# Kernel optimization log

Measured on AMD Instinct MI355X. Metric: run time of the kernel, lower is better.

## Reference

```python
import jax, jax.numpy as jnp
import numpy as np
from jax import lax

# 8-neighbor zero-pad offsets as (left, right, top, bottom), matching nn.ZeroPad2d args
PADS = [(0, 2, 0, 2), (1, 1, 0, 2), (2, 0, 0, 2), (0, 2, 1, 1),
        (2, 0, 1, 1), (0, 2, 2, 0), (1, 1, 2, 0), (2, 0, 2, 0)]
BN_EPS = 1e-5


def conv2d(x, w, pad):
    return lax.conv_general_dilated(x, w, (1, 1), [(pad, pad), (pad, pad)],
                                    dimension_numbers=('NCHW', 'OIHW', 'NCHW'))


def batchnorm(x, gamma, beta, mean, var):
    inv = gamma * lax.rsqrt(var + BN_EPS)
    return x * inv[None, :, None, None] + (beta - mean * inv)[None, :, None, None]


def resize_bilinear(x, oh, ow):
    # F.interpolate(mode='bilinear', align_corners=False)
    n, c, h, w = x.shape
    ys = jnp.clip((jnp.arange(oh, dtype=x.dtype) + 0.5) * (h / oh) - 0.5, 0.0, None)
    xs = jnp.clip((jnp.arange(ow, dtype=x.dtype) + 0.5) * (w / ow) - 0.5, 0.0, None)
    y0 = jnp.floor(ys); x0 = jnp.floor(xs)
    wy = (ys - y0)[:, None]; wx = (xs - x0)[None, :]
    y0i = jnp.clip(y0.astype(jnp.int32), 0, h - 1)
    y1i = jnp.clip(y0i + 1, 0, h - 1)
    x0i = jnp.clip(x0.astype(jnp.int32), 0, w - 1)
    x1i = jnp.clip(x0i + 1, 0, w - 1)
    r0 = x[:, :, y0i, :]; r1 = x[:, :, y1i, :]
    top = r0[:, :, :, x0i] * (1 - wx) + r0[:, :, :, x1i] * wx
    bot = r1[:, :, :, x0i] * (1 - wx) + r1[:, :, :, x1i] * wx
    return top * (1 - wy) + bot * wy


def lrwarp_error(left, disp, right):
    # Warp right image toward left using horizontal disparity (bilinear,
    # zero padding outside), then per-channel absolute photometric error.
    n, c, h, w = right.shape
    xs = jnp.arange(w, dtype=disp.dtype)[None, None, None, :] - disp  # [n,1,h,w]
    x0 = jnp.floor(xs)
    frac = xs - x0
    x0i = x0.astype(jnp.int32)
    x1i = x0i + 1
    v0 = ((x0i >= 0) & (x0i < w)).astype(right.dtype)
    v1 = ((x1i >= 0) & (x1i < w)).astype(right.dtype)
    x0c = jnp.broadcast_to(jnp.clip(x0i, 0, w - 1), (n, c, h, w))
    x1c = jnp.broadcast_to(jnp.clip(x1i, 0, w - 1), (n, c, h, w))
    g0 = jnp.take_along_axis(right, x0c, axis=3) * v0
    g1 = jnp.take_along_axis(right, x1c, axis=3) * v1
    warped = g0 * (1 - frac) + g1 * frac
    return jnp.abs(left - warped)


def setup_inputs() -> dict:
    key = jax.random.key(0)
    ks = jax.random.split(key, 16)
    N, H, W = 8, 256, 256
    inp = {
        'normal_estimation': jax.random.normal(ks[0], (N, 3, H, W), jnp.float32),
        'left_image': jax.random.uniform(ks[1], (N, 3, 512, 512), jnp.float32),
        'right_image': jax.random.uniform(ks[2], (N, 3, 512, 512), jnp.float32),
        'coarse_disparity': jax.random.uniform(ks[3], (N, 1, H, W), jnp.float32),
        'w1': jax.random.normal(ks[4], (32, 12, 3, 3), jnp.float32) * 0.1,
        'g1': jnp.ones((32,), jnp.float32), 'b1': jnp.zeros((32,), jnp.float32),
        'm1': jax.random.normal(ks[5], (32,), jnp.float32) * 0.01,
        'v1': jax.random.uniform(ks[6], (32,), jnp.float32, 0.5, 1.5),
        'w2': jax.random.normal(ks[7], (64, 32, 3, 3), jnp.float32) * 0.1,
        'g2': jnp.ones((64,), jnp.float32), 'b2': jnp.zeros((64,), jnp.float32),
        'm2': jax.random.normal(ks[8], (64,), jnp.float32) * 0.01,
        'v2': jax.random.uniform(ks[9], (64,), jnp.float32, 0.5, 1.5),
        'w3': jax.random.normal(ks[10], (8, 64, 1, 1), jnp.float32) * 0.1,
    }
    return inp


def _forward(normal_estimation, left_image, right_image, coarse_disparity,
             w1, g1, b1, m1, v1, w2, g2, b2, m2, v2, w3):
    H, W = coarse_disparity.shape[-2], coarse_disparity.shape[-1]
    cur_l = resize_bilinear(left_image, H, W)
    cur_r = resize_bilinear(right_image, H, W)
    disp_err = lrwarp_error(cur_l, coarse_disparity, cur_r)
    feats = jnp.concatenate([normal_estimation, cur_l, cur_r, disp_err], axis=1)
    x = jax.nn.relu(batchnorm(conv2d(feats, w1, 1), g1, b1, m1, v1))
    x = jax.nn.relu(batchnorm(conv2d(x, w2, 1), g2, b2, m2, v2))
    aff = jax.nn.relu(conv2d(x, w3, 0))  # [N,8,H,W]
    gate_p = jnp.stack([jnp.pad(aff[:, k], ((0, 0), (t, b), (l, r)))
                        for k, (l, r, t, b) in enumerate(PADS)], axis=1)
    d = coarse_disparity[:, 0]
    disp_p = jnp.stack([jnp.pad(d, ((0, 0), (t, b), (l, r)))
                        for (l, r, t, b) in PADS], axis=1)
    gate = jax.nn.softmax(gate_p, axis=1)
    prop = jnp.sum(gate * disp_p, axis=1, keepdims=True)[:, :, 1:-1, 1:-1]
    return prop * 0.3 + coarse_disparity * 0.7


def reference(normal_estimation, left_image, right_image, coarse_disparity,
              w1, g1, b1, m1, v1, w2, g2, b2, m2, v2, w3):
    return _forward(normal_estimation, left_image, right_image, coarse_disparity,
                    w1, g1, b1, m1, v1, w2, g2, b2, m2, v2, w3)
```

## Files before the change

kernel.cpp:

```cpp
#include <hip/hip_runtime.h>
#include <math.h>

#define NB 8
#define HH 256
#define WW 256
#define HW (HH*WW)

#define OFF_AFFB  0UL
#define OFF_W1FB  8388608UL
#define OFF_B1FB  8400896UL
#define OFF_W2FB  8401024UL
#define OFF_B2FB  8437888UL
#define OFF_W3FB  8438144UL

typedef short  short8 __attribute__((ext_vector_type(8)));
typedef ushort u16x8  __attribute__((ext_vector_type(8)));
typedef ushort u16x4  __attribute__((ext_vector_type(4)));
typedef float  f32x4  __attribute__((ext_vector_type(4)));

__device__ __forceinline__ ushort f2bf(float x) {
  uint u = __float_as_uint(x);
  return (ushort)((u + 0x7FFFu + ((u >> 16) & 1u)) >> 16);
}
__device__ __forceinline__ float bf2f(ushort h) {
  uint u = ((uint)h) << 16;
  return __uint_as_float(u);
}

__global__ __launch_bounds__(256) void prep_weights(
    const float* __restrict__ w1, const float* __restrict__ g1,
    const float* __restrict__ b1, const float* __restrict__ m1,
    const float* __restrict__ v1,
    const float* __restrict__ w2, const float* __restrict__ g2,
    const float* __restrict__ b2, const float* __restrict__ m2,
    const float* __restrict__ v2, const float* __restrict__ w3,
    char* __restrict__ wsb) {
  int idx = blockIdx.x * 256 + threadIdx.x;
  ushort* w1f = (ushort*)(wsb + OFF_W1FB);
  float* b1f  = (float*)(wsb + OFF_B1FB);
  ushort* w2f = (ushort*)(wsb + OFF_W2FB);
  float* b2f  = (float*)(wsb + OFF_B2FB);
  ushort* w3f = (ushort*)(wsb + OFF_W3FB);
  if (idx < 6144) {
    int jj = idx & 7;
    int lane = (idx >> 3) & 63;
    int nt = (idx >> 9) & 1;
    int s = idx >> 10;
    int ky = s >> 1, t = s & 1;
    int q = lane >> 4, lx = lane & 15;
    int k = q * 8 + jj;
    int dcol = k >> 4, ch = k & 15;
    int kx = t * 2 + dcol;
    int out = nt * 16 + lx;
    float inv = g1[out] / sqrtf(v1[out] + 1e-5f);
    float val = (ch < 12 && kx < 3) ? w1[((out * 12 + ch) * 3 + ky) * 3 + kx] * inv : 0.f;
    w1f[idx] = f2bf(val);
  }
  int j = idx - 6144;
  if (j >= 0 && j < 18432) {
    int kk   = j >> 11;
    int nt   = (j >> 9) & 3;
    int lane = (j >> 3) & 63;
    int jj   = j & 7;
    int q  = lane >> 4, lx = lane & 15;
    int cin = q * 8 + jj;
    int out = nt * 16 + lx;
    float inv = g2[out] / sqrtf(v2[out] + 1e-5f);
    w2f[j] = f2bf(w2[(out * 32 + cin) * 9 + kk] * inv);
    if (kk == 0 && q == 0 && jj == 0) b2f[out] = b2[out] - m2[out] * inv;
  }
  int k2 = idx - 24576;
  if (k2 >= 0 && k2 < 32) {
    float inv = g1[k2] / sqrtf(v1[k2] + 1e-5f);
    b1f[k2] = b1[k2] - m1[k2] * inv;
  }
  int k3 = idx - 24608;
  if (k3 >= 0 && k3 < 1024) {
    int jj = k3 & 7;
    int lane = (k3 >> 3) & 63;
    int slice = k3 >> 9;
    int q = lane >> 4, lx = lane & 15;
    int ch = slice * 32 + q * 8 + jj;
    w3f[k3] = (lx < 8) ? f2bf(w3[lx * 64 + ch]) : (ushort)0;
  }
}

__global__ __launch_bounds__(256) void trunk_kernel(
    const float* __restrict__ normal, const float* __restrict__ left,
    const float* __restrict__ right, const float* __restrict__ disp,
    char* __restrict__ wsb) {
  __shared__ ushort buf[18304];
  ushort* x1t = buf + 6464;
  const short8* __restrict__ w1fv = (const short8*)(wsb + OFF_W1FB);
  const float* __restrict__ b1f = (const float*)(wsb + OFF_B1FB);
  const short8* __restrict__ w2fv = (const short8*)(wsb + OFF_W2FB);
  const float* __restrict__ b2f = (const float*)(wsb + OFF_B2FB);
  const short8* __restrict__ w3fv = (const short8*)(wsb + OFF_W3FB);
  ushort* aff = (ushort*)(wsb + OFF_AFFB);

  int blk = blockIdx.x;
  int n = blk >> 8;
  int t = blk & 255;
  int ty0 = (t >> 4) << 4;
  int tx0 = (t & 15) << 4;
  int tid = threadIdx.x;
  int lane = tid & 63;
  int wid = tid >> 6;
  int q = lane >> 4;
  int lx = lane & 15;

  if (tid < 8) *(u16x8*)&buf[(800 + tid) * 8] = (u16x8)0;
  for (int e = tid; e < 400; e += 256) {
    int row = e / 20, col = e - row * 20;
    int gy = ty0 + row - 2, gx = tx0 + col - 2;
    ushort tmp[16];
#pragma unroll
    for (int c = 12; c < 16; ++c) tmp[c] = 0;
    if (gy >= 0 && gy < HH && gx >= 0 && gx < WW) {
#pragma unroll
      for (int c = 0; c < 3; ++c)
        tmp[c] = f2bf(normal[(size_t)(n * 3 + c) * HW + gy * WW + gx]);
      int i2 = gy << 1, j2 = gx << 1;
      float cl[3];
#pragma unroll
      for (int c = 0; c < 3; ++c) {
        const float* Lp = left + ((size_t)(n * 3 + c) * 512 + i2) * 512 + j2;
        float2 a0 = *(const float2*)Lp;
        float2 a1 = *(const float2*)(Lp + 512);
        cl[c] = 0.25f * (a0.x + a0.y + a1.x + a1.y);
        tmp[3 + c] = f2bf(cl[c]);
        const float* Rp = right + ((size_t)(n * 3 + c) * 512 + i2) * 512 + j2;
        float2 b0 = *(const float2*)Rp;
        float2 b1v = *(const float2*)(Rp + 512);
        tmp[6 + c] = f2bf(0.25f * (b0.x + b0.y + b1v.x + b1v.y));
      }
      float d = disp[(size_t)n * HW + gy * WW + gx];
      float xs = (float)gx - d;
      float x0f = floorf(xs);
      float fr = xs - x0f;
      int ix0 = (int)x0f;
      int ix1 = ix0 + 1;
      float vm0 = (ix0 >= 0 && ix0 < WW) ? 1.f : 0.f;
      float vm1 = (ix1 >= 0 && ix1 < WW) ? 1.f : 0.f;
      int x0c = min(max(ix0, 0), WW - 1);
      int x1c = min(max(ix1, 0), WW - 1);
      bool adj = (x1c == x0c + 1);
      int xs2 = min(x0c + 1, WW - 1);
#pragma unroll
      for (int c = 0; c < 3; ++c) {
        const float* Rb = right + ((size_t)(n * 3 + c) * 512 + i2) * 512;
        float2 f0 = *(const float2*)(Rb + (x0c << 1));
        float2 f1 = *(const float2*)(Rb + (x0c << 1) + 512);
        float2 f2v = *(const float2*)(Rb + (xs2 << 1));
        float2 f3 = *(const float2*)(Rb + (xs2 << 1) + 512);
        float avg0 = 0.25f * (f0.x + f0.y + f1.x + f1.y);
        float avg1 = 0.25f * (f2v.x + f2v.y + f3.x + f3.y);
        float gg0 = avg0 * vm0;
        float gg1 = (adj ? avg1 : avg0) * vm1;
        float warped = gg0 * (1.f - fr) + gg1 * fr;
        tmp[9 + c] = f2bf(fabsf(cl[c] - warped));
      }
    } else {
#pragma unroll
      for (int c = 0; c < 12; ++c) tmp[c] = 0;
    }
    int G0 = e * 2, G1 = G0 + 1;
    int s0 = G0 ^ ((G0 >> 3) & 7);
    int s1 = G1 ^ ((G1 >> 3) & 7);
    *(u16x8*)&buf[s0 * 8] = *(u16x8*)&tmp[0];
    *(u16x8*)&buf[s1 * 8] = *(u16x8*)&tmp[8];
  }
  __syncthreads();

  {
    short8 bw1[6][2];
#pragma unroll
    for (int s = 0; s < 6; ++s)
#pragma unroll
      for (int nt = 0; nt < 2; ++nt) bw1[s][nt] = w1fv[(s * 2 + nt) * 64 + lane];
    float bias1[2] = {b1f[lx], b1f[16 + lx]};
    for (int m = wid; m < 21; m += 4) {
      int pidx = min(m * 16 + lx, 323);
      int oyr = pidx / 18, oxr = pidx - oyr * 18;
      f32x4 a1[2];
      a1[0] = (f32x4)0.f; a1[1] = (f32x4)0.f;
#pragma unroll
      for (int s = 0; s < 6; ++s) {
        int ky = s >> 1, tt = s & 1;
        int G = ((oyr + ky) * 20 + oxr + tt * 2 + (q >> 1)) * 2 + (q & 1);
        int slot = G ^ ((G >> 3) & 7);
        short8 a = *(const short8*)&buf[slot * 8];
        a1[0] = __builtin_amdgcn_mfma_f32_16x16x32_bf16(a, bw1[s][0], a1[0], 0, 0, 0);
        a1[1] = __builtin_amdgcn_mfma_f32_16x16x32_bf16(a, bw1[s][1], a1[1], 0, 0, 0);
      }
#pragma unroll
      for (int r = 0; r < 4; ++r) {
        int p2 = m * 16 + q * 4 + r;
        if (p2 < 324) {
          int ry = p2 / 18, rx = p2 - ry * 18;
          int gy = ty0 + ry - 1, gx = tx0 + rx - 1;
          bool okp = (gy >= 0 && gy < HH && gx >= 0 && gx < WW);
#pragma unroll
          for (int nt = 0; nt < 2; ++nt) {
            float v = okp ? fmaxf(a1[nt][r] + bias1[nt], 0.f) : 0.f;
            x1t[(ry * 18 + rx) * 36 + nt * 16 + lx] = f2bf(v);
          }
        }
      }
    }
  }
  __syncthreads();

  f32x4 acc[4][4];
#pragma unroll
  for (int mt = 0; mt < 4; ++mt)
#pragma unroll
    for (int nt = 0; nt < 4; ++nt) acc[mt][nt] = (f32x4)0.f;
#pragma unroll
  for (int kk = 0; kk < 9; ++kk) {
    int ky = kk / 3, kx = kk - ky * 3;
    short8 a[4], b[4];
#pragma unroll
    for (int mt = 0; mt < 4; ++mt) {
      int row = wid * 4 + mt;
      a[mt] = *(const short8*)&x1t[((row + ky) * 18 + lx + kx) * 36 + q * 8];
    }
#pragma unroll
    for (int nt = 0; nt < 4; ++nt) b[nt] = w2fv[(kk * 4 + nt) * 64 + lane];
#pragma unroll
    for (int mt = 0; mt < 4; ++mt)
#pragma unroll
      for (int nt = 0; nt < 4; ++nt)
        acc[mt][nt] = __builtin_amdgcn_mfma_f32_16x16x32_bf16(a[mt], b[nt], acc[mt][nt], 0, 0, 0);
  }
  __syncthreads();

#pragma unroll
  for (int nt = 0; nt < 4; ++nt) {
    float bias = b2f[nt * 16 + lx];
#pragma unroll
    for (int mt = 0; mt < 4; ++mt) {
      int row = wid * 4 + mt;
#pragma unroll
      for (int r = 0; r < 4; ++r) {
        int p = row * 16 + q * 4 + r;
        float v = fmaxf(acc[mt][nt][r] + bias, 0.f);
        buf[p * 68 + nt * 16 + lx] = f2bf(v);
      }
    }
  }
  __syncthreads();

  short8 bw3[2];
  bw3[0] = w3fv[lane];
  bw3[1] = w3fv[64 + lane];
  f32x4 acc3[4];
#pragma unroll
  for (int mt = 0; mt < 4; ++mt) acc3[mt] = (f32x4)0.f;
#pragma unroll
  for (int mt = 0; mt < 4; ++mt) {
    int p = wid * 64 + mt * 16 + lx;
#pragma unroll
    for (int s = 0; s < 2; ++s) {
      short8 a3 = *(const short8*)&buf[p * 68 + s * 32 + q * 8];
      acc3[mt] = __builtin_amdgcn_mfma_f32_16x16x32_bf16(a3, bw3[s], acc3[mt], 0, 0, 0);
    }
  }
  if (lx < 8) {
#pragma unroll
    for (int mt = 0; mt < 4; ++mt) {
      int py = ty0 + wid * 4 + mt;
      int px = tx0 + q * 4;
      u16x4 pk;
#pragma unroll
      for (int r = 0; r < 4; ++r) pk[r] = f2bf(fmaxf(acc3[mt][r], 0.f));
      *(u16x4*)&aff[((size_t)(n * 8 + lx)) * HW + (size_t)py * WW + px] = pk;
    }
  }
}

__global__ __launch_bounds__(256) void final_kernel(const float* __restrict__ disp,
                                                    const char* __restrict__ wsb,
                                                    float* __restrict__ out) {
  int gid = blockIdx.x * 256 + threadIdx.x;
  int n = gid >> 14;
  int r = gid & 16383;
  int i = r >> 6;
  int j0 = (r & 63) << 2;
  const ushort* aff = (const ushort*)(wsb + OFF_AFFB);
  float d6[3][6];
#pragma unroll
  for (int rr = 0; rr < 3; ++rr) {
    int y = min(max(i + rr - 1, 0), HH - 1);
    const float* dp = disp + (size_t)n * HW + y * WW;
    float4 c4 = *(const float4*)(dp + j0);
    d6[rr][1] = c4.x; d6[rr][2] = c4.y; d6[rr][3] = c4.z; d6[rr][4] = c4.w;
    d6[rr][0] = dp[max(j0 - 1, 0)];
    d6[rr][5] = dp[min(j0 + 4, WW - 1)];
  }
  const int dy[8] = {1, 1, 1, 0, 0, -1, -1, -1};
  const int dx[8] = {1, 0, -1, 1, -1, 1, 0, -1};
  float g[8][4], dvv[8][4];
#pragma unroll
  for (int k = 0; k < 8; ++k) {
    int y = i + dy[k];
    bool vy = (y >= 0 && y < HH);
    int yc = min(max(y, 0), HH - 1);
    const ushort* ap = aff + ((size_t)(n * 8 + k)) * HW + (size_t)yc * WW;
    float w6[6];
    u16x4 c4 = *(const u16x4*)(ap + j0);
    w6[1] = bf2f(c4[0]); w6[2] = bf2f(c4[1]); w6[3] = bf2f(c4[2]); w6[4] = bf2f(c4[3]);
    w6[0] = bf2f(ap[max(j0 - 1, 0)]);
    w6[5] = bf2f(ap[min(j0 + 4, WW - 1)]);
    int rr = dy[k] + 1;
#pragma unroll
    for (int p = 0; p < 4; ++p) {
      int xp = j0 + p + dx[k];
      bool ok = vy && (xp >= 0) && (xp < WW);
      g[k][p] = ok ? w6[p + 1 + dx[k]] : 0.f;
      dvv[k][p] = ok ? d6[rr][p + 1 + dx[k]] : 0.f;
    }
  }
  float4 res;
#pragma unroll
  for (int p = 0; p < 4; ++p) {
    float m = g[0][p];
#pragma unroll
    for (int k = 1; k < 8; ++k) m = fmaxf(m, g[k][p]);
    float se = 0.f, sed = 0.f;
#pragma unroll
    for (int k = 0; k < 8; ++k) {
      float e = __expf(g[k][p] - m);
      se += e;
      sed += e * dvv[k][p];
    }
    float dc = d6[1][p + 1];
    (&res.x)[p] = 0.3f * (sed / se) + 0.7f * dc;
  }
  *(float4*)(out + (size_t)n * HW + i * WW + j0) = res;
}

extern "C" void kernel_launch(void* const* d_in, const int* in_sizes, int n_in,
                              void* d_out, int out_size, void* d_ws, size_t ws_size,
                              hipStream_t stream) {
  const float* normal = (const float*)d_in[0];
  const float* left   = (const float*)d_in[1];
  const float* right  = (const float*)d_in[2];
  const float* disp   = (const float*)d_in[3];
  const float* w1 = (const float*)d_in[4];
  const float* g1 = (const float*)d_in[5];
  const float* b1 = (const float*)d_in[6];
  const float* m1 = (const float*)d_in[7];
  const float* v1 = (const float*)d_in[8];
  const float* w2 = (const float*)d_in[9];
  const float* g2 = (const float*)d_in[10];
  const float* b2 = (const float*)d_in[11];
  const float* m2 = (const float*)d_in[12];
  const float* v2 = (const float*)d_in[13];
  const float* w3 = (const float*)d_in[14];
  char* wsb  = (char*)d_ws;
  float* out = (float*)d_out;

  hipLaunchKernelGGL(prep_weights, dim3(101), dim3(256), 0, stream,
                     w1, g1, b1, m1, v1, w2, g2, b2, m2, v2, w3, wsb);
  hipLaunchKernelGGL(trunk_kernel, dim3(2048), dim3(256), 0, stream,
                     normal, left, right, disp, wsb);
  hipLaunchKernelGGL(final_kernel, dim3(512), dim3(256), 0, stream, disp, wsb, out);
}
```

Before: 169.0 us.

## Precompute downsampled images into packed pixel-major buffer before trunk kernel

A new pass merged into the weight-prep kernel computes the 2x2-averaged left/right images and packs them with normals and disparity into a 12-float-per-pixel interleaved workspace buffer. The trunk kernel then reads three float4 per pixel instead of re-averaging the full-resolution images, including for each halo pixel and each warp gather. The goal is to cut redundant full-resolution reads and strided per-channel gathers. In exchange it adds a full write and read of an intermediate buffer of about 25 MB.

```diff
diff --git a/kernel.cpp b/kernel.cpp
--- a/kernel.cpp
+++ b/kernel.cpp
@@ -12,6 +12,7 @@
 #define OFF_W2FB  8401024UL
 #define OFF_B2FB  8437888UL
 #define OFF_W3FB  8438144UL
+#define OFF_PACK  8440192UL
 
 typedef short  short8 __attribute__((ext_vector_type(8)));
 typedef ushort u16x8  __attribute__((ext_vector_type(8)));
@@ -27,7 +28,9 @@
   return __uint_as_float(u);
 }
 
-__global__ __launch_bounds__(256) void prep_weights(
+__global__ __launch_bounds__(256) void resize_pack(
+    const float* __restrict__ normal, const float* __restrict__ left,
+    const float* __restrict__ right, const float* __restrict__ disp,
     const float* __restrict__ w1, const float* __restrict__ g1,
     const float* __restrict__ b1, const float* __restrict__ m1,
     const float* __restrict__ v1,
@@ -35,60 +38,93 @@
     const float* __restrict__ b2, const float* __restrict__ m2,
     const float* __restrict__ v2, const float* __restrict__ w3,
     char* __restrict__ wsb) {
-  int idx = blockIdx.x * 256 + threadIdx.x;
-  ushort* w1f = (ushort*)(wsb + OFF_W1FB);
-  float* b1f  = (float*)(wsb + OFF_B1FB);
-  ushort* w2f = (ushort*)(wsb + OFF_W2FB);
-  float* b2f  = (float*)(wsb + OFF_B2FB);
-  ushort* w3f = (ushort*)(wsb + OFF_W3FB);
-  if (idx < 6144) {
-    int jj = idx & 7;
-    int lane = (idx >> 3) & 63;
-    int nt = (idx >> 9) & 1;
-    int s = idx >> 10;
-    int ky = s >> 1, t = s & 1;
-    int q = lane >> 4, lx = lane & 15;
-    int k = q * 8 + jj;
-    int dcol = k >> 4, ch = k & 15;
-    int kx = t * 2 + dcol;
-    int out = nt * 16 + lx;
-    float inv = g1[out] / sqrtf(v1[out] + 1e-5f);
-    float val = (ch < 12 && kx < 3) ? w1[((out * 12 + ch) * 3 + ky) * 3 + kx] * inv : 0.f;
-    w1f[idx] = f2bf(val);
-  }
-  int j = idx - 6144;
-  if (j >= 0 && j < 18432) {
-    int kk   = j >> 11;
-    int nt   = (j >> 9) & 3;
-    int lane = (j >> 3) & 63;
-    int jj   = j & 7;
-    int q  = lane >> 4, lx = lane & 15;
-    int cin = q * 8 + jj;
-    int out = nt * 16 + lx;
-    float inv = g2[out] / sqrtf(v2[out] + 1e-5f);
-    w2f[j] = f2bf(w2[(out * 32 + cin) * 9 + kk] * inv);
-    if (kk == 0 && q == 0 && jj == 0) b2f[out] = b2[out] - m2[out] * inv;
-  }
-  int k2 = idx - 24576;
-  if (k2 >= 0 && k2 < 32) {
-    float inv = g1[k2] / sqrtf(v1[k2] + 1e-5f);
-    b1f[k2] = b1[k2] - m1[k2] * inv;
-  }
-  int k3 = idx - 24608;
-  if (k3 >= 0 && k3 < 1024) {
-    int jj = k3 & 7;
-    int lane = (k3 >> 3) & 63;
-    int slice = k3 >> 9;
-    int q = lane >> 4, lx = lane & 15;
-    int ch = slice * 32 + q * 8 + jj;
-    w3f[k3] = (lx < 8) ? f2bf(w3[lx * 64 + ch]) : (ushort)0;
-  }
-}
-
-__global__ __launch_bounds__(256) void trunk_kernel(
-    const float* __restrict__ normal, const float* __restrict__ left,
-    const float* __restrict__ right, const float* __restrict__ disp,
-    char* __restrict__ wsb) {
+  if (blockIdx.x >= 1024) {
+    int idx = (blockIdx.x - 1024) * 256 + threadIdx.x;
+    ushort* w1f = (ushort*)(wsb + OFF_W1FB);
+    float* b1f  = (float*)(wsb + OFF_B1FB);
+    ushort* w2f = (ushort*)(wsb + OFF_W2FB);
+    float* b2f  = (float*)(wsb + OFF_B2FB);
+    ushort* w3f = (ushort*)(wsb + OFF_W3FB);
+    if (idx < 6144) {
+      int jj = idx & 7;
+      int lane = (idx >> 3) & 63;
+      int nt = (idx >> 9) & 1;
+      int s = idx >> 10;
+      int ky = s >> 1, t = s & 1;
+      int q = lane >> 4, lx = lane & 15;
+      int k = q * 8 + jj;
+      int dcol = k >> 4, ch = k & 15;
+      int kx = t * 2 + dcol;
+      int out = nt * 16 + lx;
+      float inv = g1[out] / sqrtf(v1[out] + 1e-5f);
+      float val = (ch < 12 && kx < 3) ? w1[((out * 12 + ch) * 3 + ky) * 3 + kx] * inv : 0.f;
+      w1f[idx] = f2bf(val);
+    }
+    int j = idx - 6144;
+    if (j >= 0 && j < 18432) {
+      int kk   = j >> 11;
+      int nt   = (j >> 9) & 3;
+      int lane = (j >> 3) & 63;
+      int jj   = j & 7;
+      int q  = lane >> 4, lx = lane & 15;
+      int cin = q * 8 + jj;
+      int out = nt * 16 + lx;
+      float inv = g2[out] / sqrtf(v2[out] + 1e-5f);
+      w2f[j] = f2bf(w2[(out * 32 + cin) * 9 + kk] * inv);
+      if (kk == 0 && q == 0 && jj == 0) b2f[out] = b2[out] - m2[out] * inv;
+    }
+    int k2 = idx - 24576;
+    if (k2 >= 0 && k2 < 32) {
+      float inv = g1[k2] / sqrtf(v1[k2] + 1e-5f);
+      b1f[k2] = b1[k2] - m1[k2] * inv;
+    }
+    int k3 = idx - 24608;
+    if (k3 >= 0 && k3 < 1024) {
+      int jj = k3 & 7;
+      int lane = (k3 >> 3) & 63;
+      int slice = k3 >> 9;
+      int q = lane >> 4, lx = lane & 15;
+      int ch = slice * 32 + q * 8 + jj;
+      w3f[k3] = (lx < 8) ? f2bf(w3[lx * 64 + ch]) : (ushort)0;
+    }
+    return;
+  }
+  int gid = blockIdx.x * 256 + threadIdx.x;
+  int n = gid >> 15;
+  int r = gid & 32767;
+  int i = r >> 7;
+  int j0 = (r & 127) << 1;
+  int i2 = i << 1;
+  float* pack = (float*)(wsb + OFF_PACK);
+  float rec[2][12];
+#pragma unroll
+  for (int c = 0; c < 3; ++c) {
+    const float* Lp = left + ((size_t)(n * 3 + c) * 512 + i2) * 512 + (j0 << 1);
+    float4 a0 = *(const float4*)Lp;
+    float4 a1 = *(const float4*)(Lp + 512);
+    rec[0][c] = 0.25f * (a0.x + a0.y + a1.x + a1.y);
+    rec[1][c] = 0.25f * (a0.z + a0.w + a1.z + a1.w);
+    const float* Rp = right + ((size_t)(n * 3 + c) * 512 + i2) * 512 + (j0 << 1);
+    float4 b0 = *(const float4*)Rp;
+    float4 b1v = *(const float4*)(Rp + 512);
+    rec[0][3 + c] = 0.25f * (b0.x + b0.y + b1v.x + b1v.y);
+    rec[1][3 + c] = 0.25f * (b0.z + b0.w + b1v.z + b1v.w);
+    float2 nm = *(const float2*)(normal + (size_t)(n * 3 + c) * HW + i * 256 + j0);
+    rec[0][6 + c] = nm.x;
+    rec[1][6 + c] = nm.y;
+  }
+  float2 dp2 = *(const float2*)(disp + (size_t)n * HW + i * 256 + j0);
+  rec[0][9] = dp2.x; rec[1][9] = dp2.y;
+  rec[0][10] = 0.f; rec[0][11] = 0.f; rec[1][10] = 0.f; rec[1][11] = 0.f;
+  float* ob = pack + ((size_t)(n * HW + i * 256 + j0)) * 12;
+#pragma unroll
+  for (int p = 0; p < 2; ++p)
+#pragma unroll
+    for (int vv = 0; vv < 3; ++vv)
+      *(float4*)(ob + p * 12 + vv * 4) = *(float4*)&rec[p][vv * 4];
+}
+
+__global__ __launch_bounds__(256) void trunk_kernel(char* __restrict__ wsb) {
   __shared__ ushort buf[18304];
   ushort* x1t = buf + 6464;
   const short8* __restrict__ w1fv = (const short8*)(wsb + OFF_W1FB);
@@ -96,6 +132,7 @@
   const short8* __restrict__ w2fv = (const short8*)(wsb + OFF_W2FB);
   const float* __restrict__ b2f = (const float*)(wsb + OFF_B2FB);
   const short8* __restrict__ w3fv = (const short8*)(wsb + OFF_W3FB);
+  const float* __restrict__ pack = (const float*)(wsb + OFF_PACK);
   ushort* aff = (ushort*)(wsb + OFF_AFFB);
 
   int blk = blockIdx.x;
@@ -117,24 +154,16 @@
 #pragma unroll
     for (int c = 12; c < 16; ++c) tmp[c] = 0;
     if (gy >= 0 && gy < HH && gx >= 0 && gx < WW) {
-#pragma unroll
-      for (int c = 0; c < 3; ++c)
-        tmp[c] = f2bf(normal[(size_t)(n * 3 + c) * HW + gy * WW + gx]);
-      int i2 = gy << 1, j2 = gx << 1;
-      float cl[3];
-#pragma unroll
-      for (int c = 0; c < 3; ++c) {
-        const float* Lp = left + ((size_t)(n * 3 + c) * 512 + i2) * 512 + j2;
-        float2 a0 = *(const float2*)Lp;
-        float2 a1 = *(const float2*)(Lp + 512);
-        cl[c] = 0.25f * (a0.x + a0.y + a1.x + a1.y);
-        tmp[3 + c] = f2bf(cl[c]);
-        const float* Rp = right + ((size_t)(n * 3 + c) * 512 + i2) * 512 + j2;
-        float2 b0 = *(const float2*)Rp;
-        float2 b1v = *(const float2*)(Rp + 512);
-        tmp[6 + c] = f2bf(0.25f * (b0.x + b0.y + b1v.x + b1v.y));
-      }
-      float d = disp[(size_t)n * HW + gy * WW + gx];
+      const float* P = pack + ((size_t)((n << 16) + gy * 256 + gx)) * 12;
+      float4 r0 = *(const float4*)P;
+      float4 r1 = *(const float4*)(P + 4);
+      float4 r2 = *(const float4*)(P + 8);
+      float cl[3] = {r0.x, r0.y, r0.z};
+      float cr[3] = {r0.w, r1.x, r1.y};
+      tmp[0] = f2bf(r1.z); tmp[1] = f2bf(r1.w); tmp[2] = f2bf(r2.x);
+      tmp[3] = f2bf(cl[0]); tmp[4] = f2bf(cl[1]); tmp[5] = f2bf(cl[2]);
+      tmp[6] = f2bf(cr[0]); tmp[7] = f2bf(cr[1]); tmp[8] = f2bf(cr[2]);
+      float d = r2.y;
       float xs = (float)gx - d;
       float x0f = floorf(xs);
       float fr = xs - x0f;
@@ -144,20 +173,11 @@
       float vm1 = (ix1 >= 0 && ix1 < WW) ? 1.f : 0.f;
       int x0c = min(max(ix0, 0), WW - 1);
       int x1c = min(max(ix1, 0), WW - 1);
-      bool adj = (x1c == x0c + 1);
-      int xs2 = min(x0c + 1, WW - 1);
+      const float* R0 = pack + ((size_t)((n << 16) + gy * 256 + x0c)) * 12 + 3;
+      const float* R1 = pack + ((size_t)((n << 16) + gy * 256 + x1c)) * 12 + 3;
 #pragma unroll
       for (int c = 0; c < 3; ++c) {
-        const float* Rb = right + ((size_t)(n * 3 + c) * 512 + i2) * 512;
-        float2 f0 = *(const float2*)(Rb + (x0c << 1));
-        float2 f1 = *(const float2*)(Rb + (x0c << 1) + 512);
-        float2 f2v = *(const float2*)(Rb + (xs2 << 1));
-        float2 f3 = *(const float2*)(Rb + (xs2 << 1) + 512);
-        float avg0 = 0.25f * (f0.x + f0.y + f1.x + f1.y);
-        float avg1 = 0.25f * (f2v.x + f2v.y + f3.x + f3.y);
-        float gg0 = avg0 * vm0;
-        float gg1 = (adj ? avg1 : avg0) * vm1;
-        float warped = gg0 * (1.f - fr) + gg1 * fr;
+        float warped = R0[c] * vm0 * (1.f - fr) + R1[c] * vm1 * fr;
         tmp[9 + c] = f2bf(fabsf(cl[c] - warped));
       }
     } else {
@@ -361,9 +381,9 @@
   char* wsb  = (char*)d_ws;
   float* out = (float*)d_out;
 
-  hipLaunchKernelGGL(prep_weights, dim3(101), dim3(256), 0, stream,
+  hipLaunchKernelGGL(resize_pack, dim3(1125), dim3(256), 0, stream,
+                     normal, left, right, disp,
                      w1, g1, b1, m1, v1, w2, g2, b2, m2, v2, w3, wsb);
-  hipLaunchKernelGGL(trunk_kernel, dim3(2048), dim3(256), 0, stream,
-                     normal, left, right, disp, wsb);
+  hipLaunchKernelGGL(trunk_kernel, dim3(2048), dim3(256), 0, stream, wsb);
   hipLaunchKernelGGL(final_kernel, dim3(512), dim3(256), 0, stream, disp, wsb, out);
 }
```

Measured after the change: 168.4 us. About the same (-0.4%).

## Precompute bf16 feature tensor in a row kernel fused with weight prep

Applied to the files above, without the earlier changes.

Adds a per-row kernel that computes the 12-channel input features (normal, downsampled left and right images, warp error) once per pixel and stores them as bf16 in workspace. Inside that kernel the warp gathers from a shared-memory row of the downsampled right image. The weight-prep blocks are appended to the same launch. The trunk kernel now loads its halo tile straight from this feature buffer instead of recomputing features with duplicated global gathers for every halo pixel. The cost is an extra write and read of the feature tensor plus a kernel boundary in place of the fused in-tile computation.

```diff
diff --git a/kernel.cpp b/kernel.cpp
--- a/kernel.cpp
+++ b/kernel.cpp
@@ -12,6 +12,7 @@
 #define OFF_W2FB  8401024UL
 #define OFF_B2FB  8437888UL
 #define OFF_W3FB  8438144UL
+#define OFF_FEATS 8440192UL
 
 typedef short  short8 __attribute__((ext_vector_type(8)));
 typedef ushort u16x8  __attribute__((ext_vector_type(8)));
@@ -27,7 +28,9 @@
   return __uint_as_float(u);
 }
 
-__global__ __launch_bounds__(256) void prep_weights(
+__global__ __launch_bounds__(256) void feats_row(
+    const float* __restrict__ normal, const float* __restrict__ left,
+    const float* __restrict__ right, const float* __restrict__ disp,
     const float* __restrict__ w1, const float* __restrict__ g1,
     const float* __restrict__ b1, const float* __restrict__ m1,
     const float* __restrict__ v1,
@@ -35,60 +38,109 @@
     const float* __restrict__ b2, const float* __restrict__ m2,
     const float* __restrict__ v2, const float* __restrict__ w3,
     char* __restrict__ wsb) {
-  int idx = blockIdx.x * 256 + threadIdx.x;
-  ushort* w1f = (ushort*)(wsb + OFF_W1FB);
-  float* b1f  = (float*)(wsb + OFF_B1FB);
-  ushort* w2f = (ushort*)(wsb + OFF_W2FB);
-  float* b2f  = (float*)(wsb + OFF_B2FB);
-  ushort* w3f = (ushort*)(wsb + OFF_W3FB);
-  if (idx < 6144) {
-    int jj = idx & 7;
-    int lane = (idx >> 3) & 63;
-    int nt = (idx >> 9) & 1;
-    int s = idx >> 10;
-    int ky = s >> 1, t = s & 1;
-    int q = lane >> 4, lx = lane & 15;
-    int k = q * 8 + jj;
-    int dcol = k >> 4, ch = k & 15;
-    int kx = t * 2 + dcol;
-    int out = nt * 16 + lx;
-    float inv = g1[out] / sqrtf(v1[out] + 1e-5f);
-    float val = (ch < 12 && kx < 3) ? w1[((out * 12 + ch) * 3 + ky) * 3 + kx] * inv : 0.f;
-    w1f[idx] = f2bf(val);
-  }
-  int j = idx - 6144;
-  if (j >= 0 && j < 18432) {
-    int kk   = j >> 11;
-    int nt   = (j >> 9) & 3;
-    int lane = (j >> 3) & 63;
-    int jj   = j & 7;
-    int q  = lane >> 4, lx = lane & 15;
-    int cin = q * 8 + jj;
-    int out = nt * 16 + lx;
-    float inv = g2[out] / sqrtf(v2[out] + 1e-5f);
-    w2f[j] = f2bf(w2[(out * 32 + cin) * 9 + kk] * inv);
-    if (kk == 0 && q == 0 && jj == 0) b2f[out] = b2[out] - m2[out] * inv;
-  }
-  int k2 = idx - 24576;
-  if (k2 >= 0 && k2 < 32) {
-    float inv = g1[k2] / sqrtf(v1[k2] + 1e-5f);
-    b1f[k2] = b1[k2] - m1[k2] * inv;
-  }
-  int k3 = idx - 24608;
-  if (k3 >= 0 && k3 < 1024) {
-    int jj = k3 & 7;
-    int lane = (k3 >> 3) & 63;
-    int slice = k3 >> 9;
-    int q = lane >> 4, lx = lane & 15;
-    int ch = slice * 32 + q * 8 + jj;
-    w3f[k3] = (lx < 8) ? f2bf(w3[lx * 64 + ch]) : (ushort)0;
-  }
-}
-
-__global__ __launch_bounds__(256) void trunk_kernel(
-    const float* __restrict__ normal, const float* __restrict__ left,
-    const float* __restrict__ right, const float* __restrict__ disp,
-    char* __restrict__ wsb) {
+  if (blockIdx.x >= 2048) {
+    int idx = (blockIdx.x - 2048) * 256 + threadIdx.x;
+    ushort* w1f = (ushort*)(wsb + OFF_W1FB);
+    float* b1f  = (float*)(wsb + OFF_B1FB);
+    ushort* w2f = (ushort*)(wsb + OFF_W2FB);
+    float* b2f  = (float*)(wsb + OFF_B2FB);
+    ushort* w3f = (ushort*)(wsb + OFF_W3FB);
+    if (idx < 6144) {
+      int jj = idx & 7;
+      int lane = (idx >> 3) & 63;
+      int nt = (idx >> 9) & 1;
+      int s = idx >> 10;
+      int ky = s >> 1, t = s & 1;
+      int q = lane >> 4, lx = lane & 15;
+      int k = q * 8 + jj;
+      int dcol = k >> 4, ch = k & 15;
+      int kx = t * 2 + dcol;
+      int out = nt * 16 + lx;
+      float inv = g1[out] / sqrtf(v1[out] + 1e-5f);
+      float val = (ch < 12 && kx < 3) ? w1[((out * 12 + ch) * 3 + ky) * 3 + kx] * inv : 0.f;
+      w1f[idx] = f2bf(val);
+    }
+    int j = idx - 6144;
+    if (j >= 0 && j < 18432) {
+      int kk   = j >> 11;
+      int nt   = (j >> 9) & 3;
+      int lane = (j >> 3) & 63;
+      int jj   = j & 7;
+      int q  = lane >> 4, lx = lane & 15;
+      int cin = q * 8 + jj;
+      int out = nt * 16 + lx;
+      float inv = g2[out] / sqrtf(v2[out] + 1e-5f);
+      w2f[j] = f2bf(w2[(out * 32 + cin) * 9 + kk] * inv);
+      if (kk == 0 && q == 0 && jj == 0) b2f[out] = b2[out] - m2[out] * inv;
+    }
+    int k2 = idx - 24576;
+    if (k2 >= 0 && k2 < 32) {
+      float inv = g1[k2] / sqrtf(v1[k2] + 1e-5f);
+      b1f[k2] = b1[k2] - m1[k2] * inv;
+    }
+    int k3 = idx - 24608;
+    if (k3 >= 0 && k3 < 1024) {
+      int jj = k3 & 7;
+      int lane = (k3 >> 3) & 63;
+      int slice = k3 >> 9;
+      int q = lane >> 4, lx = lane & 15;
+      int ch = slice * 32 + q * 8 + jj;
+      w3f[k3] = (lx < 8) ? f2bf(w3[lx * 64 + ch]) : (ushort)0;
+    }
+    return;
+  }
+  __shared__ float curR[3][256];
+  int blk = blockIdx.x;
+  int n = blk >> 8;
+  int i = blk & 255;
+  int j = threadIdx.x;
+  int i2 = i << 1;
+  ushort* feats = (ushort*)(wsb + OFF_FEATS);
+  float cl[3], cr[3];
+#pragma unroll
+  for (int c = 0; c < 3; ++c) {
+    const float* Lp = left + ((size_t)(n * 3 + c) * 512 + i2) * 512 + (j << 1);
+    float2 a0 = *(const float2*)Lp;
+    float2 a1 = *(const float2*)(Lp + 512);
+    cl[c] = 0.25f * (a0.x + a0.y + a1.x + a1.y);
+    const float* Rp = right + ((size_t)(n * 3 + c) * 512 + i2) * 512 + (j << 1);
+    float2 b0 = *(const float2*)Rp;
+    float2 b1v = *(const float2*)(Rp + 512);
+    cr[c] = 0.25f * (b0.x + b0.y + b1v.x + b1v.y);
+    curR[c][j] = cr[c];
+  }
+  float nm[3];
+#pragma unroll
+  for (int c = 0; c < 3; ++c)
+    nm[c] = normal[(size_t)(n * 3 + c) * HW + i * WW + j];
+  float d = disp[(size_t)n * HW + i * WW + j];
+  __syncthreads();
+  float xs = (float)j - d;
+  float x0f = floorf(xs);
+  float fr = xs - x0f;
+  int ix0 = (int)x0f;
+  int ix1 = ix0 + 1;
+  float vm0 = (ix0 >= 0 && ix0 < WW) ? 1.f : 0.f;
+  float vm1 = (ix1 >= 0 && ix1 < WW) ? 1.f : 0.f;
+  int x0c = min(max(ix0, 0), WW - 1);
+  int x1c = min(max(ix1, 0), WW - 1);
+  ushort tmp[16];
+#pragma unroll
+  for (int c = 0; c < 3; ++c) {
+    float warped = curR[c][x0c] * vm0 * (1.f - fr) + curR[c][x1c] * vm1 * fr;
+    tmp[9 + c] = f2bf(fabsf(cl[c] - warped));
+    tmp[c] = f2bf(nm[c]);
+    tmp[3 + c] = f2bf(cl[c]);
+    tmp[6 + c] = f2bf(cr[c]);
+  }
+#pragma unroll
+  for (int c = 12; c < 16; ++c) tmp[c] = 0;
+  size_t ob = ((size_t)((n << 16) + i * WW + j)) * 16;
+  *(u16x8*)&feats[ob] = *(u16x8*)&tmp[0];
+  *(u16x8*)&feats[ob + 8] = *(u16x8*)&tmp[8];
+}
+
+__global__ __launch_bounds__(256) void trunk_kernel(char* __restrict__ wsb) {
   __shared__ ushort buf[18304];
   ushort* x1t = buf + 6464;
   const short8* __restrict__ w1fv = (const short8*)(wsb + OFF_W1FB);
@@ -96,6 +148,7 @@
   const short8* __restrict__ w2fv = (const short8*)(wsb + OFF_W2FB);
   const float* __restrict__ b2f = (const float*)(wsb + OFF_B2FB);
   const short8* __restrict__ w3fv = (const short8*)(wsb + OFF_W3FB);
+  const ushort* __restrict__ feats = (const ushort*)(wsb + OFF_FEATS);
   ushort* aff = (ushort*)(wsb + OFF_AFFB);
 
   int blk = blockIdx.x;
@@ -110,65 +163,17 @@
   int lx = lane & 15;
 
   if (tid < 8) *(u16x8*)&buf[(800 + tid) * 8] = (u16x8)0;
-  for (int e = tid; e < 400; e += 256) {
-    int row = e / 20, col = e - row * 20;
+  for (int e = tid; e < 800; e += 256) {
+    int row = e / 40;
+    int rem = e - row * 40;
+    int col = rem >> 1;
+    int cc = rem & 1;
     int gy = ty0 + row - 2, gx = tx0 + col - 2;
-    ushort tmp[16];
-#pragma unroll
-    for (int c = 12; c < 16; ++c) tmp[c] = 0;
-    if (gy >= 0 && gy < HH && gx >= 0 && gx < WW) {
-#pragma unroll
-      for (int c = 0; c < 3; ++c)
-        tmp[c] = f2bf(normal[(size_t)(n * 3 + c) * HW + gy * WW + gx]);
-      int i2 = gy << 1, j2 = gx << 1;
-      float cl[3];
-#pragma unroll
-      for (int c = 0; c < 3; ++c) {
-        const float* Lp = left + ((size_t)(n * 3 + c) * 512 + i2) * 512 + j2;
-        float2 a0 = *(const float2*)Lp;
-        float2 a1 = *(const float2*)(Lp + 512);
-        cl[c] = 0.25f * (a0.x + a0.y + a1.x + a1.y);
-        tmp[3 + c] = f2bf(cl[c]);
-        const float* Rp = right + ((size_t)(n * 3 + c) * 512 + i2) * 512 + j2;
-        float2 b0 = *(const float2*)Rp;
-        float2 b1v = *(const float2*)(Rp + 512);
-        tmp[6 + c] = f2bf(0.25f * (b0.x + b0.y + b1v.x + b1v.y));
-      }
-      float d = disp[(size_t)n * HW + gy * WW + gx];
-      float xs = (float)gx - d;
-      float x0f = floorf(xs);
-      float fr = xs - x0f;
-      int ix0 = (int)x0f;
-      int ix1 = ix0 + 1;
-      float vm0 = (ix0 >= 0 && ix0 < WW) ? 1.f : 0.f;
-      float vm1 = (ix1 >= 0 && ix1 < WW) ? 1.f : 0.f;
-      int x0c = min(max(ix0, 0), WW - 1);
-      int x1c = min(max(ix1, 0), WW - 1);
-      bool adj = (x1c == x0c + 1);
-      int xs2 = min(x0c + 1, WW - 1);
-#pragma unroll
-      for (int c = 0; c < 3; ++c) {
-        const float* Rb = right + ((size_t)(n * 3 + c) * 512 + i2) * 512;
-        float2 f0 = *(const float2*)(Rb + (x0c << 1));
-        float2 f1 = *(const float2*)(Rb + (x0c << 1) + 512);
-        float2 f2v = *(const float2*)(Rb + (xs2 << 1));
-        float2 f3 = *(const float2*)(Rb + (xs2 << 1) + 512);
-        float avg0 = 0.25f * (f0.x + f0.y + f1.x + f1.y);
-        float avg1 = 0.25f * (f2v.x + f2v.y + f3.x + f3.y);
-        float gg0 = avg0 * vm0;
-        float gg1 = (adj ? avg1 : avg0) * vm1;
-        float warped = gg0 * (1.f - fr) + gg1 * fr;
-        tmp[9 + c] = f2bf(fabsf(cl[c] - warped));
-      }
-    } else {
-#pragma unroll
-      for (int c = 0; c < 12; ++c) tmp[c] = 0;
-    }
-    int G0 = e * 2, G1 = G0 + 1;
-    int s0 = G0 ^ ((G0 >> 3) & 7);
-    int s1 = G1 ^ ((G1 >> 3) & 7);
-    *(u16x8*)&buf[s0 * 8] = *(u16x8*)&tmp[0];
-    *(u16x8*)&buf[s1 * 8] = *(u16x8*)&tmp[8];
+    u16x8 v = (u16x8)0;
+    if (gy >= 0 && gy < HH && gx >= 0 && gx < WW)
+      v = *(const u16x8*)&feats[((size_t)((n << 16) + gy * WW + gx)) * 16 + cc * 8];
+    int slot = e ^ ((e >> 3) & 7);
+    *(u16x8*)&buf[slot * 8] = v;
   }
   __syncthreads();
 
@@ -361,9 +366,9 @@
   char* wsb  = (char*)d_ws;
   float* out = (float*)d_out;
 
-  hipLaunchKernelGGL(prep_weights, dim3(101), dim3(256), 0, stream,
+  hipLaunchKernelGGL(feats_row, dim3(2149), dim3(256), 0, stream,
+                     normal, left, right, disp,
                      w1, g1, b1, m1, v1, w2, g2, b2, m2, v2, w3, wsb);
-  hipLaunchKernelGGL(trunk_kernel, dim3(2048), dim3(256), 0, stream,
-                     normal, left, right, disp, wsb);
+  hipLaunchKernelGGL(trunk_kernel, dim3(2048), dim3(256), 0, stream, wsb);
   hipLaunchKernelGGL(final_kernel, dim3(512), dim3(256), 0, stream, disp, wsb, out);
 }
```

New measurement: 161.5 us. -4.4%, faster.
